# Optimization experiments

Hardware: AMD Instinct MI355X
Metric: run time of the kernel (lower is better)

The kernel has to match this reference:

```python
import jax, jax.numpy as jnp
import numpy as np

B, S, IN, OUT = 16, 512, 1024, 4096
QMAX = 127.0

def setup_inputs() -> dict:
    key = jax.random.key(0)
    k1, k2, k3, k4 = jax.random.split(key, 4)
    x = jax.random.normal(k1, (B, S, IN), dtype=jnp.float32)
    # int8 weights stored as int32 spec but clamped to int8 range, cast to int8
    weight_int8 = jax.random.randint(k2, (OUT, IN), -128, 128, dtype=jnp.int32).astype(jnp.int8)
    weight_scale = jax.random.uniform(k3, (OUT,), dtype=jnp.float32, minval=1e-4, maxval=0.02)
    bias = jax.random.normal(k4, (OUT,), dtype=jnp.float32)
    return {"x": x, "weight_int8": weight_int8, "weight_scale": weight_scale, "bias": bias}

def reference(x, weight_int8, weight_scale, bias):
    # dynamic per-token abs-max quantization
    abs_max = jnp.max(jnp.abs(x), axis=-1, keepdims=True)          # [B,S,1]
    input_scale = abs_max / QMAX
    input_scale = jnp.where(input_scale == 0, 1.0, input_scale)
    x_int8 = jnp.clip(jnp.round(x / input_scale), -128.0, 127.0)   # float-emulated int8
    # int8 matmul emulated in float (as in the original F.linear on .float())
    out_i32 = jnp.einsum('bsi,oi->bso', x_int8, weight_int8.astype(jnp.float32))
    out = out_i32 * weight_scale * input_scale                     # dequantize
    out = out + bias
    return out
```

## Files before the change

### kernel.cpp

```cpp
#include <hip/hip_runtime.h>


#define M_TOT 8192
#define N_TOT 4096
#define K_TOT 1024
#define QMAXF 127.0f

#define BM 128
#define BN 128
#define BK 64
#define NKT (K_TOT / BK)

typedef int i32x4 __attribute__((ext_vector_type(4)));

__global__ __launch_bounds__(256) void prep(const float* __restrict__ x,
                                            const int* __restrict__ w32,
                                            signed char* __restrict__ xq,
                                            signed char* __restrict__ w8,
                                            float* __restrict__ iscale) {
  const int b = blockIdx.x;
  const int t = threadIdx.x;

  if (b < M_TOT) {
    const float4 v = reinterpret_cast<const float4*>(x)[(size_t)b * 256 + t];
    float m = fmaxf(fmaxf(fabsf(v.x), fabsf(v.y)), fmaxf(fabsf(v.z), fabsf(v.w)));
#pragma unroll
    for (int off = 32; off >= 1; off >>= 1) m = fmaxf(m, __shfl_xor(m, off, 64));

    __shared__ float wmax[4];
    const int lane = t & 63, wid = t >> 6;
    if (lane == 0) wmax[wid] = m;
    __syncthreads();
    const float amax = fmaxf(fmaxf(wmax[0], wmax[1]), fmaxf(wmax[2], wmax[3]));

    float scale = amax / QMAXF;
    if (scale == 0.0f) scale = 1.0f;

    int qi;
    signed char* qb = reinterpret_cast<signed char*>(&qi);
    qb[0] = (signed char)(int)fminf(fmaxf(rintf(v.x / scale), -128.0f), 127.0f);
    qb[1] = (signed char)(int)fminf(fmaxf(rintf(v.y / scale), -128.0f), 127.0f);
    qb[2] = (signed char)(int)fminf(fmaxf(rintf(v.z / scale), -128.0f), 127.0f);
    qb[3] = (signed char)(int)fminf(fmaxf(rintf(v.w / scale), -128.0f), 127.0f);
    reinterpret_cast<int*>(xq)[(size_t)b * 256 + t] = qi;

    if (t == 0) iscale[b] = scale;
  } else {
    const int i = (b - M_TOT) * 256 + t;
    const int4 v = reinterpret_cast<const int4*>(w32)[i];
    const int packed = (v.x & 0xFF) | ((v.y & 0xFF) << 8) |
                       ((v.z & 0xFF) << 16) | (v.w << 24);
    reinterpret_cast<int*>(w8)[i] = packed;
  }
}

__device__ __forceinline__ void gload_lds16(const void* g, void* l) {
  __builtin_amdgcn_global_load_lds(
      (const __attribute__((address_space(1))) unsigned int*)g,
      (__attribute__((address_space(3))) unsigned int*)l, 16, 0, 0);
}

__global__ __launch_bounds__(256, 4) void int8_gemm(const signed char* __restrict__ xq,
                                                    const signed char* __restrict__ w,
                                                    const float* __restrict__ iscale,
                                                    const float* __restrict__ wscale,
                                                    const float* __restrict__ bias,
                                                    float* __restrict__ out) {
  __shared__ __attribute__((aligned(16))) signed char As[2][BM][BK];
  __shared__ __attribute__((aligned(16))) signed char Bs[2][BN][BK];

  const int t = threadIdx.x;
  const int lane = t & 63;
  const int wid = t >> 6;
  const int wm = wid >> 1;
  const int wn = wid & 1;

  const int bid = blockIdx.x;
  const int xcd = bid & 7, li = bid >> 3;
  const int mt = (xcd >> 1) * 16 + (li >> 4);
  const int nt = (xcd & 1) * 16 + (li & 15);
  const int m0 = mt * BM, n0 = nt * BN;

  const int srow = t >> 2;
  const int scol_swz = ((t & 3) * 16) ^ (((srow >> 1) & 3) << 4);

  auto stage = [&](int buf, int kt) {
    const int k0 = kt * BK;
#pragma unroll
    for (int c = 0; c < 2; ++c) {
      gload_lds16(xq + (size_t)(m0 + c * 64 + srow) * K_TOT + k0 + scol_swz,
                  &As[buf][c * 64][0] + t * 16);
      gload_lds16(w + (size_t)(n0 + c * 64 + srow) * K_TOT + k0 + scol_swz,
                  &Bs[buf][c * 64][0] + t * 16);
    }
  };

  const int lr = lane & 15;
  const int kq = (lane >> 4) * 16;
  auto rdA = [&](int buf, int f) -> i32x4 {
    const int r = wm * 64 + f * 16 + lr;
    return *reinterpret_cast<const i32x4*>(&As[buf][r][kq ^ (((r >> 1) & 3) << 4)]);
  };
  auto rdB = [&](int buf, int g) -> i32x4 {
    const int r = wn * 64 + g * 16 + lr;
    return *reinterpret_cast<const i32x4*>(&Bs[buf][r][kq ^ (((r >> 1) & 3) << 4)]);
  };

  i32x4 acc[4][4] = {};

  stage(0, 0);
  __syncthreads();

  for (int kt = 0; kt < NKT; ++kt) {
    const int cur = kt & 1;
    if (kt + 1 < NKT) stage(cur ^ 1, kt + 1);

    i32x4 a[4], b[4];
#pragma unroll
    for (int f = 0; f < 4; ++f) a[f] = rdA(cur, f);
#pragma unroll
    for (int g = 0; g < 4; ++g) b[g] = rdB(cur, g);

    __builtin_amdgcn_s_setprio(1);
#pragma unroll
    for (int f = 0; f < 4; ++f)
#pragma unroll
      for (int g = 0; g < 4; ++g)
        acc[f][g] = __builtin_amdgcn_mfma_i32_16x16x64_i8(a[f], b[g], acc[f][g], 0, 0, 0);
    __builtin_amdgcn_s_setprio(0);

    __syncthreads();
  }

  const int col = lane & 15;
  const int rq = lane >> 4;
  float wsc[4], bv[4];
#pragma unroll
  for (int g = 0; g < 4; ++g) {
    const int gn = n0 + wn * 64 + g * 16 + col;
    wsc[g] = wscale[gn];
    bv[g] = bias[gn];
  }
#pragma unroll
  for (int f = 0; f < 4; ++f) {
    const int gmb = m0 + wm * 64 + f * 16 + rq * 4;
#pragma unroll
    for (int i = 0; i < 4; ++i) {
      const int gm = gmb + i;
      const float isc = iscale[gm];
      float* rowp = out + (size_t)gm * N_TOT + n0 + wn * 64 + col;
#pragma unroll
      for (int g = 0; g < 4; ++g)
        rowp[g * 16] = (float)acc[f][g][i] * wsc[g] * isc + bv[g];
    }
  }
}

extern "C" void kernel_launch(void* const* d_in, const int* in_sizes, int n_in,
                              void* d_out, int out_size, void* d_ws, size_t ws_size,
                              hipStream_t stream) {
  const float* x = (const float*)d_in[0];
  const int* w32 = (const int*)d_in[1];
  const float* wscale = (const float*)d_in[2];
  const float* bias = (const float*)d_in[3];
  float* out = (float*)d_out;

  signed char* xq = (signed char*)d_ws;
  float* iscale = (float*)((char*)d_ws + (size_t)M_TOT * K_TOT);
  signed char* w8 = (signed char*)((char*)d_ws + (size_t)M_TOT * K_TOT + M_TOT * 4);

  const int pack_blocks = (N_TOT * K_TOT / 4) / 256;
  prep<<<M_TOT + pack_blocks, 256, 0, stream>>>(x, w32, xq, w8, iscale);
  int8_gemm<<<dim3((M_TOT / BM) * (N_TOT / BN)), 256, 0, stream>>>(xq, w8, iscale, wscale, bias, out);
}
```

Measured before the change: 68.67 us.

## Warp-specialize int8 GEMM with dedicated loader wave and BK=128 tiles

Adds a fifth wave per block that only issues global-to-LDS loads into a double buffer. The four compute waves only read LDS and issue MFMAs, synchronised by raw s_barrier instructions. The K tile doubles to 128, which halves the number of barriers, and the per-row input scales are hoisted into registers before the main loop. The goal is to take load issue off the compute waves' critical path. In exchange, LDS use per block doubles, occupancy drops from 4 to 2 blocks per CU, and a single wave must sustain the full load bandwidth.

```diff
diff --git a/kernel.cpp b/kernel.cpp
--- a/kernel.cpp
+++ b/kernel.cpp
@@ -8,7 +8,7 @@
 
 #define BM 128
 #define BN 128
-#define BK 64
+#define BK 128
 #define NKT (K_TOT / BK)
 
 typedef int i32x4 __attribute__((ext_vector_type(4)));
@@ -60,7 +60,9 @@
       (__attribute__((address_space(3))) unsigned int*)l, 16, 0, 0);
 }
 
-__global__ __launch_bounds__(256, 4) void int8_gemm(const signed char* __restrict__ xq,
+#define BARF asm volatile("s_barrier" ::: "memory")
+
+__global__ __launch_bounds__(320, 2) void int8_gemm(const signed char* __restrict__ xq,
                                                     const signed char* __restrict__ w,
                                                     const float* __restrict__ iscale,
                                                     const float* __restrict__ wscale,
@@ -72,8 +74,6 @@
   const int t = threadIdx.x;
   const int lane = t & 63;
   const int wid = t >> 6;
-  const int wm = wid >> 1;
-  const int wn = wid & 1;
 
   const int bid = blockIdx.x;
   const int xcd = bid & 7, li = bid >> 3;
@@ -81,56 +81,46 @@
   const int nt = (xcd & 1) * 16 + (li & 15);
   const int m0 = mt * BM, n0 = nt * BN;
 
-  const int srow = t >> 2;
-  const int scol_swz = ((t & 3) * 16) ^ (((srow >> 1) & 3) << 4);
+  if (wid == 4) {
+    const int srow = lane >> 3;
+    const int ssw = ((lane & 7) * 16) ^ (srow << 4);
 
-  auto stage = [&](int buf, int kt) {
-    const int k0 = kt * BK;
+    auto stg = [&](int buf, int kt) {
+      const int k0 = kt * BK;
 #pragma unroll
-    for (int c = 0; c < 2; ++c) {
-      gload_lds16(xq + (size_t)(m0 + c * 64 + srow) * K_TOT + k0 + scol_swz,
-                  &As[buf][c * 64][0] + t * 16);
-      gload_lds16(w + (size_t)(n0 + c * 64 + srow) * K_TOT + k0 + scol_swz,
-                  &Bs[buf][c * 64][0] + t * 16);
+      for (int c = 0; c < 16; ++c)
+        gload_lds16(xq + (size_t)(m0 + c * 8 + srow) * K_TOT + k0 + ssw,
+                    &As[buf][c * 8][0]);
+#pragma unroll
+      for (int c = 0; c < 16; ++c)
+        gload_lds16(w + (size_t)(n0 + c * 8 + srow) * K_TOT + k0 + ssw,
+                    &Bs[buf][c * 8][0]);
+    };
+
+    stg(0, 0);
+    asm volatile("s_waitcnt vmcnt(0)" ::: "memory");
+    BARF;
+    for (int k2 = 0; k2 < NKT - 1; ++k2) {
+      stg((k2 + 1) & 1, k2 + 1);
+      asm volatile("s_waitcnt vmcnt(0)" ::: "memory");
+      BARF;
     }
-  };
+    return;
+  }
 
+  const int wm = wid >> 1;
+  const int wn = wid & 1;
   const int lr = lane & 15;
   const int kq = (lane >> 4) * 16;
-  auto rdA = [&](int buf, int f) -> i32x4 {
+
+  auto rdA = [&](int buf, int f, int ks) -> i32x4 {
     const int r = wm * 64 + f * 16 + lr;
-    return *reinterpret_cast<const i32x4*>(&As[buf][r][kq ^ (((r >> 1) & 3) << 4)]);
+    return *reinterpret_cast<const i32x4*>(&As[buf][r][(ks * 64 + kq) ^ ((r & 7) << 4)]);
   };
-  auto rdB = [&](int buf, int g) -> i32x4 {
+  auto rdB = [&](int buf, int g, int ks) -> i32x4 {
     const int r = wn * 64 + g * 16 + lr;
-    return *reinterpret_cast<const i32x4*>(&Bs[buf][r][kq ^ (((r >> 1) & 3) << 4)]);
+    return *reinterpret_cast<const i32x4*>(&Bs[buf][r][(ks * 64 + kq) ^ ((r & 7) << 4)]);
   };
-
-  i32x4 acc[4][4] = {};
-
-  stage(0, 0);
-  __syncthreads();
-
-  for (int kt = 0; kt < NKT; ++kt) {
-    const int cur = kt & 1;
-    if (kt + 1 < NKT) stage(cur ^ 1, kt + 1);
-
-    i32x4 a[4], b[4];
-#pragma unroll
-    for (int f = 0; f < 4; ++f) a[f] = rdA(cur, f);
-#pragma unroll
-    for (int g = 0; g < 4; ++g) b[g] = rdB(cur, g);
-
-    __builtin_amdgcn_s_setprio(1);
-#pragma unroll
-    for (int f = 0; f < 4; ++f)
-#pragma unroll
-      for (int g = 0; g < 4; ++g)
-        acc[f][g] = __builtin_amdgcn_mfma_i32_16x16x64_i8(a[f], b[g], acc[f][g], 0, 0, 0);
-    __builtin_amdgcn_s_setprio(0);
-
-    __syncthreads();
-  }
 
   const int col = lane & 15;
   const int rq = lane >> 4;
@@ -141,17 +131,48 @@
     wsc[g] = wscale[gn];
     bv[g] = bias[gn];
   }
+  float isc[4][4];
+#pragma unroll
+  for (int f = 0; f < 4; ++f)
+#pragma unroll
+    for (int i = 0; i < 4; ++i)
+      isc[f][i] = iscale[m0 + wm * 64 + f * 16 + rq * 4 + i];
+
+  i32x4 acc[4][4] = {};
+
+  for (int k2 = 0; k2 < NKT; ++k2) {
+    const int c = k2 & 1;
+    BARF;
+    i32x4 a[4][2], b[4][2];
+#pragma unroll
+    for (int ks = 0; ks < 2; ++ks) {
+#pragma unroll
+      for (int f = 0; f < 4; ++f) a[f][ks] = rdA(c, f, ks);
+#pragma unroll
+      for (int g = 0; g < 4; ++g) b[g][ks] = rdB(c, g, ks);
+    }
+    __builtin_amdgcn_s_setprio(1);
+#pragma unroll
+    for (int ks = 0; ks < 2; ++ks)
+#pragma unroll
+      for (int f = 0; f < 4; ++f)
+#pragma unroll
+        for (int g = 0; g < 4; ++g)
+          acc[f][g] = __builtin_amdgcn_mfma_i32_16x16x64_i8(a[f][ks], b[g][ks],
+                                                            acc[f][g], 0, 0, 0);
+    __builtin_amdgcn_s_setprio(0);
+  }
+
 #pragma unroll
   for (int f = 0; f < 4; ++f) {
     const int gmb = m0 + wm * 64 + f * 16 + rq * 4;
 #pragma unroll
     for (int i = 0; i < 4; ++i) {
       const int gm = gmb + i;
-      const float isc = iscale[gm];
       float* rowp = out + (size_t)gm * N_TOT + n0 + wn * 64 + col;
 #pragma unroll
       for (int g = 0; g < 4; ++g)
-        rowp[g * 16] = (float)acc[f][g][i] * wsc[g] * isc + bv[g];
+        rowp[g * 16] = (float)acc[f][g][i] * wsc[g] * isc[f][i] + bv[g];
     }
   }
 }
@@ -171,5 +192,5 @@
 
   const int pack_blocks = (N_TOT * K_TOT / 4) / 256;
   prep<<<M_TOT + pack_blocks, 256, 0, stream>>>(x, w32, xq, w8, iscale);
-  int8_gemm<<<dim3((M_TOT / BM) * (N_TOT / BN)), 256, 0, stream>>>(xq, w8, iscale, wscale, bias, out);
+  int8_gemm<<<dim3((M_TOT / BM) * (N_TOT / BN)), 320, 0, stream>>>(xq, w8, iscale, wscale, bias, out);
 }
```

Result: slower. 76.05 us (+10.7%).
